# Kernel optimization log

Hardware: AMD Instinct MI355X
Metric: run time of the kernel (lower is better)

The kernel has to match this reference:

```python
import jax, jax.numpy as jnp
import numpy as np

N = 50000   # nodes
E = 400000  # edges per metapath
M = 3       # metapaths
L = 2       # HAN layers
IN = 256    # input feat = hidden*heads so layers stack
H = 4       # heads
DO = 64     # out per head
D = H * DO  # 256


def setup_inputs() -> dict:
    key = jax.random.key(0)
    ks = jax.random.split(key, 12)
    x = jax.random.normal(ks[0], (M, N, IN), jnp.float32)
    src = jax.random.randint(ks[1], (M, E), 0, N, jnp.int32)
    dst = jax.random.randint(ks[2], (M, E), 0, N, jnp.int32)
    W_gat = jax.random.normal(ks[3], (L, M, IN, D), jnp.float32) * 0.06
    attn_l = jax.random.normal(ks[4], (L, M, H, DO), jnp.float32) * 0.1
    attn_r = jax.random.normal(ks[5], (L, M, H, DO), jnp.float32) * 0.1
    bias_gat = jnp.zeros((L, M, D), jnp.float32)
    W1 = jax.random.normal(ks[6], (D, DO), jnp.float32) * 0.06
    b1 = jnp.zeros((DO,), jnp.float32)
    W2 = jax.random.normal(ks[7], (DO, 1), jnp.float32) * 0.1
    Wp = jax.random.normal(ks[8], (D, DO), jnp.float32) * 0.06
    bp = jnp.zeros((DO,), jnp.float32)
    return {"x": x, "W_gat": W_gat, "attn_l": attn_l, "attn_r": attn_r,
            "bias_gat": bias_gat, "W1": W1, "b1": b1, "W2": W2,
            "Wp": Wp, "bp": bp, "src": src, "dst": dst}


def gat_conv(h, src, dst, W, al, ar, bias):
    # h: (N, IN) -> feat: (N, H, DO)
    feat = (h @ W).reshape(N, H, DO)
    el = jnp.einsum('nhd,hd->nh', feat, al)   # (N, H)
    er = jnp.einsum('nhd,hd->nh', feat, ar)   # (N, H)
    e = jax.nn.leaky_relu(el[src] + er[dst], 0.2)  # (E, H)
    # numerically stable edge softmax over incoming edges per dst node
    mx = jax.ops.segment_max(e, dst, num_segments=N)  # (N, H)
    mx = jnp.where(jnp.isfinite(mx), mx, 0.0)         # empty segments
    ex = jnp.exp(e - mx[dst])                         # (E, H)
    denom = jax.ops.segment_sum(ex, dst, num_segments=N)  # (N, H)
    msg = jax.ops.segment_sum(ex[:, :, None] * feat[src], dst, num_segments=N)  # (N,H,DO)
    out = msg / jnp.maximum(denom, 1e-9)[:, :, None]
    out = out + bias.reshape(H, DO)
    return jax.nn.elu(out).reshape(N, D)  # flatten(1)


def reference(x, W_gat, attn_l, attn_r, bias_gat, W1, b1, W2, Wp, bp, src, dst):
    h = [x[i] for i in range(M)]
    for l in range(L):
        h = [gat_conv(h[i], src[i], dst[i], W_gat[l, i], attn_l[l, i],
                      attn_r[l, i], bias_gat[l, i]) for i in range(M)]
    z = jnp.stack(h, axis=1)  # (N, M, D)
    # semantic attention: small MLP -> per-metapath scalar, softmax over M
    w = (jnp.tanh(z @ W1 + b1) @ W2).mean(0)   # (M, 1)
    beta = jax.nn.softmax(w, axis=0)           # (M, 1)
    agg = (z * beta[None]).sum(1)              # (N, D)
    return agg @ Wp + bp                       # (N, DO)
```

## Files before the change

### kernel.cpp

```cpp
#include <hip/hip_runtime.h>

#define NN 50000
#define EE 400000
#define MM 3
#define CHUNK 2048
#define NCHUNK ((NN + CHUNK - 1) / CHUNK)

typedef float f32x4 __attribute__((ext_vector_type(4)));
typedef short s16x8 __attribute__((ext_vector_type(8)));
typedef _Float16 half_t;
typedef _Float16 h16x4 __attribute__((ext_vector_type(4)));

union FU { float f; unsigned u; };

__device__ inline short bfhi(float x) {
    FU c; c.f = x;
    unsigned u = c.u;
    return (short)((u + 0x7fffu + ((u >> 16) & 1u)) >> 16);
}
__device__ inline float bf2f(short h) {
    FU c; c.u = ((unsigned)(unsigned short)h) << 16;
    return c.f;
}
__device__ inline float h2f(short bits) {
    union HU { short s; _Float16 h; } u; u.s = bits; return (float)u.h;
}


__global__ __launch_bounds__(256) void init_kernel(int* counts, float* wsum) {
    int idx = blockIdx.x * 256 + threadIdx.x;
    if (idx < MM * NN) counts[idx] = 0;
    if (idx < MM) wsum[idx] = 0.0f;
}

__global__ __launch_bounds__(256) void hist_kernel(const int* __restrict__ dst,
                                                   int* __restrict__ counts) {
    int m = blockIdx.y;
    int e = blockIdx.x * 256 + threadIdx.x;
    if (e < EE) atomicAdd(&counts[m * NN + dst[m * EE + e]], 1);
}

__global__ __launch_bounds__(256) void scan_partial_kernel(const int* __restrict__ counts,
                                                           int* __restrict__ rp,
                                                           int* __restrict__ bsum) {
    int m = blockIdx.y, ch = blockIdx.x;
    const int* c = counts + m * NN;
    int* r = rp + m * (NN + 1);
    int t = threadIdx.x, lane = t & 63, wave = t >> 6;
    int i0 = ch * CHUNK + t * 8;
    int v[8]; int s = 0;
#pragma unroll
    for (int k = 0; k < 8; ++k) { int i = i0 + k; v[k] = (i < NN) ? c[i] : 0; s += v[k]; }
    int incl = s;
#pragma unroll
    for (int off = 1; off < 64; off <<= 1) {
        int u = __shfl_up(incl, off);
        if (lane >= off) incl += u;
    }
    int excl = incl - s;
    __shared__ int wsh[4];
    if (lane == 63) wsh[wave] = incl;
    __syncthreads();
    int woff = 0;
    for (int w = 0; w < wave; ++w) woff += wsh[w];
    int run = excl + woff;
#pragma unroll
    for (int k = 0; k < 8; ++k) { int i = i0 + k; if (i < NN) r[i] = run; run += v[k]; }
    if (t == 255) bsum[m * NCHUNK + ch] = woff + incl;
}

__global__ __launch_bounds__(256) void scan_top_kernel(int* __restrict__ bsum) {
    int wave = threadIdx.x >> 6, lane = threadIdx.x & 63;
    if (wave < MM) {
        int v = (lane < NCHUNK) ? bsum[wave * NCHUNK + lane] : 0;
        int incl = v;
#pragma unroll
        for (int off = 1; off < 64; off <<= 1) {
            int u = __shfl_up(incl, off);
            if (lane >= off) incl += u;
        }
        if (lane < NCHUNK) bsum[wave * NCHUNK + lane] = incl - v;
    }
}

__global__ __launch_bounds__(256) void scan_add_kernel(const int* __restrict__ bsum,
                                                       int* __restrict__ rp,
                                                       int* __restrict__ cur) {
    int m = blockIdx.y, ch = blockIdx.x;
    int off = bsum[m * NCHUNK + ch];
    int* r = rp + m * (NN + 1);
    int* q = cur + m * (NN + 1);
    int i0 = ch * CHUNK + threadIdx.x * 8;
#pragma unroll
    for (int k = 0; k < 8; ++k) {
        int i = i0 + k;
        if (i < NN) { int val = r[i] + off; r[i] = val; q[i] = val; }
    }
    if (ch == 0 && threadIdx.x == 0) r[NN] = EE;
}

__global__ __launch_bounds__(256) void scatter_kernel(const int* __restrict__ src,
                                                      const int* __restrict__ dst,
                                                      int* __restrict__ cursor,
                                                      long long* __restrict__ spair) {
    int m = blockIdx.y;
    int e = blockIdx.x * 256 + threadIdx.x;
    if (e < EE) {
        int d = dst[m * EE + e];
        int pos = atomicAdd(&cursor[m * (NN + 1) + d], 1);
        long long p = ((long long)d << 32) | (unsigned)src[m * EE + e];
        __builtin_nontemporal_store(p, &spair[(size_t)m * EE + pos]);
    }
}


#define WG_ELEMS (6 * 256 * 256)
#define W_TOT (WG_ELEMS + 128 * 256)

__global__ __launch_bounds__(256) void splitW_kernel(const float* __restrict__ Wg,
                                                     const float* __restrict__ W1,
                                                     const float* __restrict__ Wp,
                                                     short* __restrict__ Whi,
                                                     short* __restrict__ Wlo) {
    int idx = blockIdx.x * 256 + threadIdx.x;
    if (idx >= W_TOT) return;
    float v;
    if (idx < WG_ELEMS) {
        int mat = idx >> 16, rem = idx & 65535;
        int n = rem >> 8, k = rem & 255;
        v = Wg[mat * 65536 + k * 256 + n];
    } else {
        int i2 = idx - WG_ELEMS;
        int n = i2 >> 8, k = i2 & 255;
        v = (n < 64) ? W1[k * 64 + n] : Wp[k * 64 + n - 64];
    }
    short h = bfhi(v);
    Whi[idx] = h;
    Wlo[idx] = bfhi(v - bf2f(h));
}


template<int AMODE>
__global__ __launch_bounds__(256) void mfma_gemm(
    const float* __restrict__ Af, const half_t* __restrict__ A16,
    const short* __restrict__ Wthi, const short* __restrict__ Wtlo,
    half_t* __restrict__ featA,
    const float* __restrict__ alA, const float* __restrict__ arA,
    float* __restrict__ elA, float* __restrict__ erA) {
    __shared__ short Ah[64 * 32], Al[64 * 32], Bh[256 * 32], Bl[256 * 32];
    const int m = blockIdx.y;
    const int t = threadIdx.x;
    const int lane = t & 63;
    const int wn = t >> 6;
    const int row0 = blockIdx.x * 64;
    const float*  A0 = Af + (size_t)m * NN * 256;
    const short*  A1 = (const short*)(A16 + (size_t)m * NN * 256);
    const short*  Bgh = Wthi + (size_t)m * 65536;
    const short*  Bgl = Wtlo + (size_t)m * 65536;
    half_t* Ch = featA + (size_t)m * NN * 256;
    const float* al = alA + m * 256;
    const float* ar = arA + m * 256;
    float* el = elA + (size_t)m * NN * 4;
    float* er = erA + (size_t)m * NN * 4;
    f32x4 acc[4][4] = {};

    const int r = t >> 2, c0 = t & 3;
    const int aoff = r * 32 + ((c0 ^ ((r >> 1) & 3)) << 3);
    const int arow = row0 + r;
    const bool aval = (arow < NN);

    s16x8 praw = {0,0,0,0,0,0,0,0};
    float4 pf0 = make_float4(0.f,0.f,0.f,0.f), pf1 = make_float4(0.f,0.f,0.f,0.f);

    if (AMODE == 1) {
        if (aval) praw = *(const s16x8*)(A1 + (size_t)arow * 256 + c0 * 8);
    } else {
        if (aval) {
            pf0 = *(const float4*)(A0 + (size_t)arow * 256 + c0 * 8);
            pf1 = *(const float4*)(A0 + (size_t)arow * 256 + c0 * 8 + 4);
        }
    }

    for (int k0 = 0; k0 < 256; k0 += 32) {
        {
            float v[8];
            if (AMODE == 1) {
#pragma unroll
                for (int j = 0; j < 8; ++j) v[j] = h2f(praw[j]);
            } else {
                v[0] = pf0.x; v[1] = pf0.y; v[2] = pf0.z; v[3] = pf0.w;
                v[4] = pf1.x; v[5] = pf1.y; v[6] = pf1.z; v[7] = pf1.w;
            }
            s16x8 hh, ll;
#pragma unroll
            for (int j = 0; j < 8; ++j) {
                short hs = bfhi(v[j]);
                hh[j] = hs;
                ll[j] = bfhi(v[j] - bf2f(hs));
            }
            *(s16x8*)&Ah[aoff] = hh;
            *(s16x8*)&Al[aoff] = ll;
        }
#pragma unroll
        for (int u = 0; u < 4; ++u) {
            int n = u * 64 + (t >> 2), c = t & 3;
            s16x8 h = *(const s16x8*)(Bgh + (size_t)n * 256 + k0 + c * 8);
            s16x8 l = *(const s16x8*)(Bgl + (size_t)n * 256 + k0 + c * 8);
            int off = n * 32 + ((c ^ ((n >> 1) & 3)) << 3);
            *(s16x8*)&Bh[off] = h;
            *(s16x8*)&Bl[off] = l;
        }
        __syncthreads();
        if (k0 + 32 < 256) {
            if (AMODE == 1) {
                praw = s16x8{0,0,0,0,0,0,0,0};
                if (aval) praw = *(const s16x8*)(A1 + (size_t)arow * 256 + k0 + 32 + c0 * 8);
            } else {
                pf0 = make_float4(0.f,0.f,0.f,0.f); pf1 = make_float4(0.f,0.f,0.f,0.f);
                if (aval) {
                    pf0 = *(const float4*)(A0 + (size_t)arow * 256 + k0 + 32 + c0 * 8);
                    pf1 = *(const float4*)(A0 + (size_t)arow * 256 + k0 + 32 + c0 * 8 + 4);
                }
            }
        }
        int fr = lane & 15, ac = lane >> 4;
        s16x8 afh[4], afl[4], bfh[4], bfl[4];
#pragma unroll
        for (int i = 0; i < 4; ++i) {
            int rr = i * 16 + fr;
            int off = rr * 32 + ((ac ^ ((rr >> 1) & 3)) << 3);
            afh[i] = *(const s16x8*)&Ah[off];
            afl[i] = *(const s16x8*)&Al[off];
        }
#pragma unroll
        for (int j = 0; j < 4; ++j) {
            int n = wn * 64 + j * 16 + fr;
            int off = n * 32 + ((ac ^ ((n >> 1) & 3)) << 3);
            bfh[j] = *(const s16x8*)&Bh[off];
            bfl[j] = *(const s16x8*)&Bl[off];
        }
#pragma unroll
        for (int i = 0; i < 4; ++i)
#pragma unroll
            for (int j = 0; j < 4; ++j) {
                acc[i][j] = __builtin_amdgcn_mfma_f32_16x16x32_bf16(afh[i], bfh[j], acc[i][j], 0, 0, 0);
                acc[i][j] = __builtin_amdgcn_mfma_f32_16x16x32_bf16(afh[i], bfl[j], acc[i][j], 0, 0, 0);
                acc[i][j] = __builtin_amdgcn_mfma_f32_16x16x32_bf16(afl[i], bfh[j], acc[i][j], 0, 0, 0);
            }
        __syncthreads();
    }

#pragma unroll
    for (int i = 0; i < 4; ++i) {
        int rbase = row0 + i * 16 + (lane >> 4) * 4;
#pragma unroll
        for (int j = 0; j < 4; ++j) {
            int col = wn * 64 + j * 16 + (lane & 15);
#pragma unroll
            for (int q = 0; q < 4; ++q) {
                int row = rbase + q;
                if (row < NN) Ch[(size_t)row * 256 + col] = (half_t)acc[i][j][q];
            }
        }
    }
    float alv[4], arv[4];
#pragma unroll
    for (int j = 0; j < 4; ++j) {
        int col = wn * 64 + j * 16 + (lane & 15);
        alv[j] = al[col];
        arv[j] = ar[col];
    }
#pragma unroll
    for (int i = 0; i < 4; ++i)
#pragma unroll
        for (int q = 0; q < 4; ++q) {
            float ep = acc[i][0][q] * alv[0] + acc[i][1][q] * alv[1]
                     + acc[i][2][q] * alv[2] + acc[i][3][q] * alv[3];
            float rp_ = acc[i][0][q] * arv[0] + acc[i][1][q] * arv[1]
                      + acc[i][2][q] * arv[2] + acc[i][3][q] * arv[3];
#pragma unroll
            for (int msk = 1; msk < 16; msk <<= 1) {
                ep += __shfl_xor(ep, msk);
                rp_ += __shfl_xor(rp_, msk);
            }
            if ((lane & 15) == 0) {
                int row = row0 + i * 16 + (lane >> 4) * 4 + q;
                if (row < NN) {
                    el[row * 4 + wn] = ep;
                    er[row * 4 + wn] = rp_;
                }
            }
        }
}


__global__ __launch_bounds__(256) void sem_gemm(
    const half_t* __restrict__ A16,
    const short* __restrict__ Wthi, const short* __restrict__ Wtlo,
    float* __restrict__ P,
    const float* __restrict__ b1, const float* __restrict__ w2,
    float* __restrict__ wsum,
    int nrows) {
    __shared__ short Ah[128 * 32], Al[128 * 32], Bh[128 * 32], Bl[128 * 32];
    const int t = threadIdx.x;
    const int lane = t & 63;
    const int wave = t >> 6;
    const int wm = wave >> 1, wn = wave & 1;
    const int row0 = blockIdx.x * 128;
    const short* A1 = (const short*)A16;
    f32x4 acc[4][4] = {};

    const int r0 = (t * 2) >> 2, c0 = (t * 2) & 3;
    const int r1 = (t * 2 + 1) >> 2, c1 = (t * 2 + 1) & 3;
    const int aoff0 = r0 * 32 + ((c0 ^ ((r0 >> 1) & 3)) << 3);
    const int aoff1 = r1 * 32 + ((c1 ^ ((r1 >> 1) & 3)) << 3);
    const int arow0 = row0 + r0, arow1 = row0 + r1;

    s16x8 p0 = {0,0,0,0,0,0,0,0}, p1 = {0,0,0,0,0,0,0,0};
    if (arow0 < nrows) p0 = *(const s16x8*)(A1 + (size_t)arow0 * 256 + c0 * 8);
    if (arow1 < nrows) p1 = *(const s16x8*)(A1 + (size_t)arow1 * 256 + c1 * 8);

    for (int k0 = 0; k0 < 256; k0 += 32) {
        {
            s16x8 hh, ll;
#pragma unroll
            for (int j = 0; j < 8; ++j) {
                float v = h2f(p0[j]);
                short hs = bfhi(v);
                hh[j] = hs; ll[j] = bfhi(v - bf2f(hs));
            }
            *(s16x8*)&Ah[aoff0] = hh; *(s16x8*)&Al[aoff0] = ll;
#pragma unroll
            for (int j = 0; j < 8; ++j) {
                float v = h2f(p1[j]);
                short hs = bfhi(v);
                hh[j] = hs; ll[j] = bfhi(v - bf2f(hs));
            }
            *(s16x8*)&Ah[aoff1] = hh; *(s16x8*)&Al[aoff1] = ll;
        }
#pragma unroll
        for (int u = 0; u < 2; ++u) {
            int idx = t * 2 + u;
            int n = idx >> 2, c = idx & 3;
            s16x8 h = *(const s16x8*)(Wthi + (size_t)n * 256 + k0 + c * 8);
            s16x8 l = *(const s16x8*)(Wtlo + (size_t)n * 256 + k0 + c * 8);
            int off = n * 32 + ((c ^ ((n >> 1) & 3)) << 3);
            *(s16x8*)&Bh[off] = h;
            *(s16x8*)&Bl[off] = l;
        }
        __syncthreads();
        if (k0 + 32 < 256) {
            p0 = s16x8{0,0,0,0,0,0,0,0}; p1 = s16x8{0,0,0,0,0,0,0,0};
            if (arow0 < nrows) p0 = *(const s16x8*)(A1 + (size_t)arow0 * 256 + k0 + 32 + c0 * 8);
            if (arow1 < nrows) p1 = *(const s16x8*)(A1 + (size_t)arow1 * 256 + k0 + 32 + c1 * 8);
        }
        int fr = lane & 15, ac = lane >> 4;
        s16x8 afh[4], afl[4], bfh[4], bfl[4];
#pragma unroll
        for (int i = 0; i < 4; ++i) {
            int rr = wm * 64 + i * 16 + fr;
            int off = rr * 32 + ((ac ^ ((rr >> 1) & 3)) << 3);
            afh[i] = *(const s16x8*)&Ah[off];
            afl[i] = *(const s16x8*)&Al[off];
        }
#pragma unroll
        for (int j = 0; j < 4; ++j) {
            int n = wn * 64 + j * 16 + fr;
            int off = n * 32 + ((ac ^ ((n >> 1) & 3)) << 3);
            bfh[j] = *(const s16x8*)&Bh[off];
            bfl[j] = *(const s16x8*)&Bl[off];
        }
#pragma unroll
        for (int i = 0; i < 4; ++i)
#pragma unroll
            for (int j = 0; j < 4; ++j) {
                acc[i][j] = __builtin_amdgcn_mfma_f32_16x16x32_bf16(afh[i], bfh[j], acc[i][j], 0, 0, 0);
                acc[i][j] = __builtin_amdgcn_mfma_f32_16x16x32_bf16(afh[i], bfl[j], acc[i][j], 0, 0, 0);
                acc[i][j] = __builtin_amdgcn_mfma_f32_16x16x32_bf16(afl[i], bfh[j], acc[i][j], 0, 0, 0);
            }
        __syncthreads();
    }

    float* wp = (float*)&Ah[0];
    if (t < 3) wp[t] = 0.f;
    __syncthreads();
    int fr = lane & 15, ac = lane >> 4;
    if (wn == 0) {
        float b1v[4], w2v[4];
#pragma unroll
        for (int j = 0; j < 4; ++j) {
            int col = j * 16 + fr;
            b1v[j] = b1[col];
            w2v[j] = w2[col];
        }
#pragma unroll
        for (int i = 0; i < 4; ++i)
#pragma unroll
            for (int q = 0; q < 4; ++q) {
                float ep = tanhf(acc[i][0][q] + b1v[0]) * w2v[0]
                         + tanhf(acc[i][1][q] + b1v[1]) * w2v[1]
                         + tanhf(acc[i][2][q] + b1v[2]) * w2v[2]
                         + tanhf(acc[i][3][q] + b1v[3]) * w2v[3];
#pragma unroll
                for (int msk = 1; msk < 16; msk <<= 1) ep += __shfl_xor(ep, msk);
                if (fr == 0) {
                    int row = row0 + wm * 64 + i * 16 + ac * 4 + q;
                    if (row < nrows) atomicAdd(&wp[row / NN], ep);
                }
            }
    } else {
#pragma unroll
        for (int i = 0; i < 4; ++i) {
            int rbase = row0 + wm * 64 + i * 16 + ac * 4;
#pragma unroll
            for (int j = 0; j < 4; ++j) {
                int pcol = j * 16 + fr;
#pragma unroll
                for (int q = 0; q < 4; ++q) {
                    int row = rbase + q;
                    if (row < nrows) P[(size_t)row * 64 + pcol] = acc[i][j][q];
                }
            }
        }
    }
    __syncthreads();
    if (t < 3) atomicAdd(&wsum[t], wp[t]);
}


__global__ __launch_bounds__(256) void edge_w_kernel(const long long* __restrict__ spairA,
                                                     const float* __restrict__ elA,
                                                     const float* __restrict__ erA,
                                                     float* __restrict__ wTA) {
    const int m = blockIdx.y;
    int j = blockIdx.x * 256 + threadIdx.x;
    if (j >= EE) return;
    long long p = spairA[(size_t)m * EE + j];
    int s = (int)(unsigned)(p & 0xffffffffLL);
    int d = (int)(p >> 32);
    const float4 e_l = ((const float4*)(elA + (size_t)m * NN * 4))[s];
    const float4 e_r = ((const float4*)(erA + (size_t)m * NN * 4))[d];
    float* wT = wTA + (size_t)m * 4 * EE;
    float e0 = e_l.x + e_r.x; e0 = e0 > 0.f ? e0 : 0.2f * e0;
    float e1 = e_l.y + e_r.y; e1 = e1 > 0.f ? e1 : 0.2f * e1;
    float e2 = e_l.z + e_r.z; e2 = e2 > 0.f ? e2 : 0.2f * e2;
    float e3 = e_l.w + e_r.w; e3 = e3 > 0.f ? e3 : 0.2f * e3;
    wT[0 * EE + j] = __expf(e0);
    wT[1 * EE + j] = __expf(e1);
    wT[2 * EE + j] = __expf(e2);
    wT[3 * EE + j] = __expf(e3);
}


__global__ __launch_bounds__(256) void agg_edges_kernel(const half_t* __restrict__ featA,
                                                        const float* __restrict__ wTA,
                                                        const long long* __restrict__ spairA,
                                                        const int* __restrict__ row_ptrA,
                                                        const float* __restrict__ biasL,
                                                        half_t* __restrict__ HbA) {
    const int m = blockIdx.y;
    const half_t* feat = featA + (size_t)m * NN * 256;
    const int* row_ptr = row_ptrA + (size_t)m * (NN + 1);
    const long long* spair = spairA + (size_t)m * EE;
    const float* bias = biasL + m * 256;
    half_t* out = HbA + (size_t)m * NN * 256;

    int wave = threadIdx.x >> 6;
    int lane = threadIdx.x & 63;
    int n = blockIdx.x * 4 + wave;
    int h = lane >> 4;
    const float* wh = wTA + (size_t)m * 4 * EE + (size_t)h * EE;
    int beg = row_ptr[n], end = row_ptr[n + 1];
    const h16x4* fb = (const h16x4*)feat + lane;
    float a0A = 0.f, a1A = 0.f, a2A = 0.f, a3A = 0.f, dA = 0.f;
    float a0B = 0.f, a1B = 0.f, a2B = 0.f, a3B = 0.f, dB = 0.f;
    float a0C = 0.f, a1C = 0.f, a2C = 0.f, a3C = 0.f, dC = 0.f;
    float a0D = 0.f, a1D = 0.f, a2D = 0.f, a3D = 0.f, dD = 0.f;
    int j = beg;
    for (; j + 3 < end; j += 4) {
        int sA = (int)(unsigned)spair[j];
        int sB = (int)(unsigned)spair[j + 1];
        int sC = (int)(unsigned)spair[j + 2];
        int sD = (int)(unsigned)spair[j + 3];
        float wA = wh[j], wB = wh[j + 1], wC = wh[j + 2], wD = wh[j + 3];
        h16x4 fA = fb[(size_t)sA * 64];
        h16x4 fB = fb[(size_t)sB * 64];
        h16x4 fC = fb[(size_t)sC * 64];
        h16x4 fD = fb[(size_t)sD * 64];
        a0A = fmaf(wA, (float)fA.x, a0A); a1A = fmaf(wA, (float)fA.y, a1A);
        a2A = fmaf(wA, (float)fA.z, a2A); a3A = fmaf(wA, (float)fA.w, a3A); dA += wA;
        a0B = fmaf(wB, (float)fB.x, a0B); a1B = fmaf(wB, (float)fB.y, a1B);
        a2B = fmaf(wB, (float)fB.z, a2B); a3B = fmaf(wB, (float)fB.w, a3B); dB += wB;
        a0C = fmaf(wC, (float)fC.x, a0C); a1C = fmaf(wC, (float)fC.y, a1C);
        a2C = fmaf(wC, (float)fC.z, a2C); a3C = fmaf(wC, (float)fC.w, a3C); dC += wC;
        a0D = fmaf(wD, (float)fD.x, a0D); a1D = fmaf(wD, (float)fD.y, a1D);
        a2D = fmaf(wD, (float)fD.z, a2D); a3D = fmaf(wD, (float)fD.w, a3D); dD += wD;
    }
    for (; j < end; ++j) {
        int s = (int)(unsigned)spair[j];
        float w = wh[j];
        h16x4 f = fb[(size_t)s * 64];
        a0A = fmaf(w, (float)f.x, a0A); a1A = fmaf(w, (float)f.y, a1A);
        a2A = fmaf(w, (float)f.z, a2A); a3A = fmaf(w, (float)f.w, a3A); dA += w;
    }
    float den = fmaxf((dA + dB) + (dC + dD), 1e-9f);
    int col = lane * 4;
    float o0 = ((a0A + a0B) + (a0C + a0D)) / den + bias[col + 0];
    float o1 = ((a1A + a1B) + (a1C + a1D)) / den + bias[col + 1];
    float o2 = ((a2A + a2B) + (a2C + a2D)) / den + bias[col + 2];
    float o3 = ((a3A + a3B) + (a3C + a3D)) / den + bias[col + 3];
    o0 = o0 > 0.f ? o0 : __expf(o0) - 1.0f;
    o1 = o1 > 0.f ? o1 : __expf(o1) - 1.0f;
    o2 = o2 > 0.f ? o2 : __expf(o2) - 1.0f;
    o3 = o3 > 0.f ? o3 : __expf(o3) - 1.0f;
    h16x4 ov; ov.x = (half_t)o0; ov.y = (half_t)o1; ov.z = (half_t)o2; ov.w = (half_t)o3;
    ((h16x4*)(out + (size_t)n * 256))[lane] = ov;
}


__global__ void beta_kernel(const float* __restrict__ wsum, float* __restrict__ beta) {
    if (threadIdx.x == 0 && blockIdx.x == 0) {
        float w0 = wsum[0] / (float)NN, w1 = wsum[1] / (float)NN, w2 = wsum[2] / (float)NN;
        float mx = fmaxf(w0, fmaxf(w1, w2));
        float e0 = __expf(w0 - mx), e1 = __expf(w1 - mx), e2 = __expf(w2 - mx);
        float s = e0 + e1 + e2;
        beta[0] = e0 / s; beta[1] = e1 / s; beta[2] = e2 / s;
    }
}

__global__ __launch_bounds__(256) void combine_out_kernel(const float* __restrict__ P,
                                                          const float* __restrict__ beta,
                                                          const float* __restrict__ bp,
                                                          float* __restrict__ out) {
    int idx4 = blockIdx.x * 256 + threadIdx.x;
    if (idx4 >= NN * 64 / 4) return;
    float b0 = beta[0], b1 = beta[1], b2 = beta[2];
    float4 p0 = ((const float4*)P)[idx4];
    float4 p1 = ((const float4*)P)[idx4 + NN * 16];
    float4 p2 = ((const float4*)P)[idx4 + NN * 32];
    float4 bpv = *(const float4*)(bp + ((idx4 * 4) & 63));
    float4 o;
    o.x = b0 * p0.x + b1 * p1.x + b2 * p2.x + bpv.x;
    o.y = b0 * p0.y + b1 * p1.y + b2 * p2.y + bpv.y;
    o.z = b0 * p0.z + b1 * p1.z + b2 * p2.z + bpv.z;
    o.w = b0 * p0.w + b1 * p1.w + b2 * p2.w + bpv.w;
    ((float4*)out)[idx4] = o;
}


extern "C" void kernel_launch(void* const* d_in, const int* in_sizes, int n_in,
                              void* d_out, int out_size, void* d_ws, size_t ws_size,
                              hipStream_t stream) {
    const float* x        = (const float*)d_in[0];
    const float* W_gat    = (const float*)d_in[1];
    const float* attn_l   = (const float*)d_in[2];
    const float* attn_r   = (const float*)d_in[3];
    const float* bias_gat = (const float*)d_in[4];
    const float* W1       = (const float*)d_in[5];
    const float* b1       = (const float*)d_in[6];
    const float* W2       = (const float*)d_in[7];
    const float* Wp       = (const float*)d_in[8];
    const float* bp       = (const float*)d_in[9];
    const int*   src      = (const int*)d_in[10];
    const int*   dst      = (const int*)d_in[11];
    float* out = (float*)d_out;

    char* ws = (char*)d_ws;
    size_t off = 0;
    auto alloc = [&](size_t bytes) { size_t o = off; off = (off + bytes + 255) & ~(size_t)255; return o; };
    half_t* Hb      = (half_t*)(ws + alloc((size_t)MM * NN * 256 * 2));
    half_t* feat    = (half_t*)(ws + alloc((size_t)MM * NN * 256 * 2));
    float*  P       = (float*)(ws + alloc((size_t)MM * NN * 64 * 4));
    float*  el      = (float*)(ws + alloc((size_t)MM * NN * 4 * 4));
    float*  er      = (float*)(ws + alloc((size_t)MM * NN * 4 * 4));
    int*    counts  = (int*)(ws + alloc((size_t)MM * NN * 4));
    int*    row_ptr = (int*)(ws + alloc((size_t)MM * (NN + 1) * 4));
    int*    cursor  = (int*)(ws + alloc((size_t)MM * (NN + 1) * 4));
    long long* spair = (long long*)(ws + alloc((size_t)MM * EE * 8));
    float*  wT      = (float*)(ws + alloc((size_t)MM * 4 * EE * 4));
    int*    bsum    = (int*)(ws + alloc((size_t)MM * NCHUNK * 4));
    short*  Whi     = (short*)(ws + alloc((size_t)W_TOT * 2));
    short*  Wlo     = (short*)(ws + alloc((size_t)W_TOT * 2));
    float*  wsum    = (float*)(ws + alloc(16));
    float*  beta    = (float*)(ws + alloc(16));

    init_kernel<<<dim3((MM * NN + 255) / 256), 256, 0, stream>>>(counts, wsum);
    hist_kernel<<<dim3((EE + 255) / 256, MM), 256, 0, stream>>>(dst, counts);
    scan_partial_kernel<<<dim3(NCHUNK, MM), 256, 0, stream>>>(counts, row_ptr, bsum);
    scan_top_kernel<<<dim3(1), 256, 0, stream>>>(bsum);
    scan_add_kernel<<<dim3(NCHUNK, MM), 256, 0, stream>>>(bsum, row_ptr, cursor);
    scatter_kernel<<<dim3((EE + 255) / 256, MM), 256, 0, stream>>>(src, dst, cursor, spair);
    splitW_kernel<<<dim3((W_TOT + 255) / 256), 256, 0, stream>>>(W_gat, W1, Wp, Whi, Wlo);

    const int rowTiles = (NN + 63) / 64;

    for (int l = 0; l < 2; ++l) {
        const short* wh = Whi + (size_t)l * MM * 65536;
        const short* wl = Wlo + (size_t)l * MM * 65536;
        const float* alp = attn_l + (size_t)l * MM * 256;
        const float* arp = attn_r + (size_t)l * MM * 256;
        if (l == 0)
            mfma_gemm<0><<<dim3(rowTiles, MM), 256, 0, stream>>>(
                x, nullptr, wh, wl, feat, alp, arp, el, er);
        else
            mfma_gemm<1><<<dim3(rowTiles, MM), 256, 0, stream>>>(
                nullptr, Hb, wh, wl, feat, alp, arp, el, er);
        edge_w_kernel<<<dim3((EE + 255) / 256, MM), 256, 0, stream>>>(spair, el, er, wT);
        agg_edges_kernel<<<dim3(NN / 4, MM), 256, 0, stream>>>(
            feat, wT, spair, row_ptr, bias_gat + (size_t)l * MM * 256, Hb);
    }

    sem_gemm<<<dim3((MM * NN + 127) / 128), 256, 0, stream>>>(
        Hb, Whi + WG_ELEMS, Wlo + WG_ELEMS, P, b1, W2, wsum, MM * NN);
    beta_kernel<<<dim3(1), 64, 0, stream>>>(wsum, beta);
    combine_out_kernel<<<dim3((NN * 16 + 255) / 256), 256, 0, stream>>>(P, beta, bp, out);
}
```

Baseline: 682.7 us.

## Fuse edge weight computation into aggregation and use direct-to-LDS weight loads in GEMM

Removes the separate edge_w_kernel and its wT buffer; the aggregation kernel now recomputes the leaky-relu and exp edge weights from el/er for each gathered source. Each weight is computed 16 times per wave, once per lane of a head, but the global write and read of wT disappear. In the GEMM, the weight matrices are pre-swizzled into the LDS tile layout so B tiles can be copied with global_load_lds, bypassing registers. A-operand prefetch is deepened to two k-blocks ahead.

```diff
diff --git a/kernel.cpp b/kernel.cpp
--- a/kernel.cpp
+++ b/kernel.cpp
@@ -24,6 +24,12 @@
 }
 __device__ inline float h2f(short bits) {
     union HU { short s; _Float16 h; } u; u.s = bits; return (float)u.h;
+}
+
+__device__ inline void glds16(const void* g, void* l) {
+    __builtin_amdgcn_global_load_lds(
+        (const __attribute__((address_space(1))) void*)g,
+        (__attribute__((address_space(3))) void*)l, 16, 0, 0);
 }
 
 
@@ -126,8 +132,16 @@
     if (idx >= W_TOT) return;
     float v;
     if (idx < WG_ELEMS) {
-        int mat = idx >> 16, rem = idx & 65535;
-        int n = rem >> 8, k = rem & 255;
+        int mat = idx >> 16;
+        int rem = idx & 65535;
+        int kb  = rem >> 13;
+        int r2  = rem & 8191;
+        int n   = r2 >> 5;
+        int s5  = r2 & 31;
+        int cc  = s5 >> 3;
+        int jj  = s5 & 7;
+        int c   = cc ^ ((n >> 1) & 3);
+        int k   = kb * 32 + c * 8 + jj;
         v = Wg[mat * 65536 + k * 256 + n];
     } else {
         int i2 = idx - WG_ELEMS;
@@ -155,8 +169,8 @@
     const int row0 = blockIdx.x * 64;
     const float*  A0 = Af + (size_t)m * NN * 256;
     const short*  A1 = (const short*)(A16 + (size_t)m * NN * 256);
-    const short*  Bgh = Wthi + (size_t)m * 65536;
-    const short*  Bgl = Wtlo + (size_t)m * 65536;
+    const char*   BghB = (const char*)(Wthi + (size_t)m * 65536);
+    const char*   BglB = (const char*)(Wtlo + (size_t)m * 65536);
     half_t* Ch = featA + (size_t)m * NN * 256;
     const float* al = alA + m * 256;
     const float* ar = arA + m * 256;
@@ -168,28 +182,34 @@
     const int aoff = r * 32 + ((c0 ^ ((r >> 1) & 3)) << 3);
     const int arow = row0 + r;
     const bool aval = (arow < NN);
-
-    s16x8 praw = {0,0,0,0,0,0,0,0};
-    float4 pf0 = make_float4(0.f,0.f,0.f,0.f), pf1 = make_float4(0.f,0.f,0.f,0.f);
+    const int cb = wn * 4096;
+
+    s16x8 pr0 = {0,0,0,0,0,0,0,0}, pr1 = {0,0,0,0,0,0,0,0};
+    float4 a00 = make_float4(0.f,0.f,0.f,0.f), a01 = a00, a10 = a00, a11 = a00;
 
     if (AMODE == 1) {
-        if (aval) praw = *(const s16x8*)(A1 + (size_t)arow * 256 + c0 * 8);
+        if (aval) {
+            pr0 = *(const s16x8*)(A1 + (size_t)arow * 256 + c0 * 8);
+            pr1 = *(const s16x8*)(A1 + (size_t)arow * 256 + 32 + c0 * 8);
+        }
     } else {
         if (aval) {
-            pf0 = *(const float4*)(A0 + (size_t)arow * 256 + c0 * 8);
-            pf1 = *(const float4*)(A0 + (size_t)arow * 256 + c0 * 8 + 4);
-        }
-    }
-
-    for (int k0 = 0; k0 < 256; k0 += 32) {
+            a00 = *(const float4*)(A0 + (size_t)arow * 256 + c0 * 8);
+            a01 = *(const float4*)(A0 + (size_t)arow * 256 + c0 * 8 + 4);
+            a10 = *(const float4*)(A0 + (size_t)arow * 256 + 32 + c0 * 8);
+            a11 = *(const float4*)(A0 + (size_t)arow * 256 + 32 + c0 * 8 + 4);
+        }
+    }
+
+    for (int kb = 0; kb < 8; ++kb) {
         {
             float v[8];
             if (AMODE == 1) {
 #pragma unroll
-                for (int j = 0; j < 8; ++j) v[j] = h2f(praw[j]);
+                for (int j = 0; j < 8; ++j) v[j] = h2f(pr0[j]);
             } else {
-                v[0] = pf0.x; v[1] = pf0.y; v[2] = pf0.z; v[3] = pf0.w;
-                v[4] = pf1.x; v[5] = pf1.y; v[6] = pf1.z; v[7] = pf1.w;
+                v[0] = a00.x; v[1] = a00.y; v[2] = a00.z; v[3] = a00.w;
+                v[4] = a01.x; v[5] = a01.y; v[6] = a01.z; v[7] = a01.w;
             }
             s16x8 hh, ll;
 #pragma unroll
@@ -201,28 +221,31 @@
             *(s16x8*)&Ah[aoff] = hh;
             *(s16x8*)&Al[aoff] = ll;
         }
-#pragma unroll
-        for (int u = 0; u < 4; ++u) {
-            int n = u * 64 + (t >> 2), c = t & 3;
-            s16x8 h = *(const s16x8*)(Bgh + (size_t)n * 256 + k0 + c * 8);
-            s16x8 l = *(const s16x8*)(Bgl + (size_t)n * 256 + k0 + c * 8);
-            int off = n * 32 + ((c ^ ((n >> 1) & 3)) << 3);
-            *(s16x8*)&Bh[off] = h;
-            *(s16x8*)&Bl[off] = l;
+        if (AMODE == 1) {
+            pr0 = pr1;
+            pr1 = s16x8{0,0,0,0,0,0,0,0};
+            if (kb + 2 < 8 && aval)
+                pr1 = *(const s16x8*)(A1 + (size_t)arow * 256 + (kb + 2) * 32 + c0 * 8);
+        } else {
+            a00 = a10; a01 = a11;
+            a10 = make_float4(0.f,0.f,0.f,0.f); a11 = a10;
+            if (kb + 2 < 8 && aval) {
+                a10 = *(const float4*)(A0 + (size_t)arow * 256 + (kb + 2) * 32 + c0 * 8);
+                a11 = *(const float4*)(A0 + (size_t)arow * 256 + (kb + 2) * 32 + c0 * 8 + 4);
+            }
+        }
+        {
+            const char* sh = BghB + kb * 16384 + cb;
+            const char* sl = BglB + kb * 16384 + cb;
+            char* dh = (char*)&Bh[0] + cb;
+            char* dl = (char*)&Bl[0] + cb;
+#pragma unroll
+            for (int u = 0; u < 4; ++u) {
+                glds16(sh + u * 1024 + lane * 16, dh + u * 1024);
+                glds16(sl + u * 1024 + lane * 16, dl + u * 1024);
+            }
         }
         __syncthreads();
-        if (k0 + 32 < 256) {
-            if (AMODE == 1) {
-                praw = s16x8{0,0,0,0,0,0,0,0};
-                if (aval) praw = *(const s16x8*)(A1 + (size_t)arow * 256 + k0 + 32 + c0 * 8);
-            } else {
-                pf0 = make_float4(0.f,0.f,0.f,0.f); pf1 = make_float4(0.f,0.f,0.f,0.f);
-                if (aval) {
-                    pf0 = *(const float4*)(A0 + (size_t)arow * 256 + k0 + 32 + c0 * 8);
-                    pf1 = *(const float4*)(A0 + (size_t)arow * 256 + k0 + 32 + c0 * 8 + 4);
-                }
-            }
-        }
         int fr = lane & 15, ac = lane >> 4;
         s16x8 afh[4], afl[4], bfh[4], bfl[4];
 #pragma unroll
@@ -428,38 +451,17 @@
 }
 
 
-__global__ __launch_bounds__(256) void edge_w_kernel(const long long* __restrict__ spairA,
-                                                     const float* __restrict__ elA,
-                                                     const float* __restrict__ erA,
-                                                     float* __restrict__ wTA) {
-    const int m = blockIdx.y;
-    int j = blockIdx.x * 256 + threadIdx.x;
-    if (j >= EE) return;
-    long long p = spairA[(size_t)m * EE + j];
-    int s = (int)(unsigned)(p & 0xffffffffLL);
-    int d = (int)(p >> 32);
-    const float4 e_l = ((const float4*)(elA + (size_t)m * NN * 4))[s];
-    const float4 e_r = ((const float4*)(erA + (size_t)m * NN * 4))[d];
-    float* wT = wTA + (size_t)m * 4 * EE;
-    float e0 = e_l.x + e_r.x; e0 = e0 > 0.f ? e0 : 0.2f * e0;
-    float e1 = e_l.y + e_r.y; e1 = e1 > 0.f ? e1 : 0.2f * e1;
-    float e2 = e_l.z + e_r.z; e2 = e2 > 0.f ? e2 : 0.2f * e2;
-    float e3 = e_l.w + e_r.w; e3 = e3 > 0.f ? e3 : 0.2f * e3;
-    wT[0 * EE + j] = __expf(e0);
-    wT[1 * EE + j] = __expf(e1);
-    wT[2 * EE + j] = __expf(e2);
-    wT[3 * EE + j] = __expf(e3);
-}
-
-
 __global__ __launch_bounds__(256) void agg_edges_kernel(const half_t* __restrict__ featA,
-                                                        const float* __restrict__ wTA,
+                                                        const float* __restrict__ elA,
+                                                        const float* __restrict__ erA,
+                                                        const int* __restrict__ row_ptrA,
                                                         const long long* __restrict__ spairA,
-                                                        const int* __restrict__ row_ptrA,
                                                         const float* __restrict__ biasL,
                                                         half_t* __restrict__ HbA) {
     const int m = blockIdx.y;
     const half_t* feat = featA + (size_t)m * NN * 256;
+    const float* el = elA + (size_t)m * NN * 4;
+    const float* er = erA + (size_t)m * NN * 4;
     const int* row_ptr = row_ptrA + (size_t)m * (NN + 1);
     const long long* spair = spairA + (size_t)m * EE;
     const float* bias = biasL + m * 256;
@@ -469,8 +471,8 @@
     int lane = threadIdx.x & 63;
     int n = blockIdx.x * 4 + wave;
     int h = lane >> 4;
-    const float* wh = wTA + (size_t)m * 4 * EE + (size_t)h * EE;
     int beg = row_ptr[n], end = row_ptr[n + 1];
+    float ern = er[n * 4 + h];
     const h16x4* fb = (const h16x4*)feat + lane;
     float a0A = 0.f, a1A = 0.f, a2A = 0.f, a3A = 0.f, dA = 0.f;
     float a0B = 0.f, a1B = 0.f, a2B = 0.f, a3B = 0.f, dB = 0.f;
@@ -482,7 +484,10 @@
         int sB = (int)(unsigned)spair[j + 1];
         int sC = (int)(unsigned)spair[j + 2];
         int sD = (int)(unsigned)spair[j + 3];
-        float wA = wh[j], wB = wh[j + 1], wC = wh[j + 2], wD = wh[j + 3];
+        float eA = el[sA * 4 + h] + ern; eA = eA > 0.f ? eA : 0.2f * eA; float wA = __expf(eA);
+        float eB = el[sB * 4 + h] + ern; eB = eB > 0.f ? eB : 0.2f * eB; float wB = __expf(eB);
+        float eC = el[sC * 4 + h] + ern; eC = eC > 0.f ? eC : 0.2f * eC; float wC = __expf(eC);
+        float eD = el[sD * 4 + h] + ern; eD = eD > 0.f ? eD : 0.2f * eD; float wD = __expf(eD);
         h16x4 fA = fb[(size_t)sA * 64];
         h16x4 fB = fb[(size_t)sB * 64];
         h16x4 fC = fb[(size_t)sC * 64];
@@ -498,7 +503,9 @@
     }
     for (; j < end; ++j) {
         int s = (int)(unsigned)spair[j];
-        float w = wh[j];
+        float e = el[s * 4 + h] + ern;
+        e = e > 0.f ? e : 0.2f * e;
+        float w = __expf(e);
         h16x4 f = fb[(size_t)s * 64];
         a0A = fmaf(w, (float)f.x, a0A); a1A = fmaf(w, (float)f.y, a1A);
         a2A = fmaf(w, (float)f.z, a2A); a3A = fmaf(w, (float)f.w, a3A); dA += w;
@@ -577,7 +584,6 @@
     int*    row_ptr = (int*)(ws + alloc((size_t)MM * (NN + 1) * 4));
     int*    cursor  = (int*)(ws + alloc((size_t)MM * (NN + 1) * 4));
     long long* spair = (long long*)(ws + alloc((size_t)MM * EE * 8));
-    float*  wT      = (float*)(ws + alloc((size_t)MM * 4 * EE * 4));
     int*    bsum    = (int*)(ws + alloc((size_t)MM * NCHUNK * 4));
     short*  Whi     = (short*)(ws + alloc((size_t)W_TOT * 2));
     short*  Wlo     = (short*)(ws + alloc((size_t)W_TOT * 2));
@@ -605,9 +611,8 @@
         else
             mfma_gemm<1><<<dim3(rowTiles, MM), 256, 0, stream>>>(
                 nullptr, Hb, wh, wl, feat, alp, arp, el, er);
-        edge_w_kernel<<<dim3((EE + 255) / 256, MM), 256, 0, stream>>>(spair, el, er, wT);
         agg_edges_kernel<<<dim3(NN / 4, MM), 256, 0, stream>>>(
-            feat, wT, spair, row_ptr, bias_gat + (size_t)l * MM * 256, Hb);
+            feat, el, er, row_ptr, spair, bias_gat + (size_t)l * MM * 256, Hb);
     }
 
     sem_gemm<<<dim3((MM * NN + 127) / 128), 256, 0, stream>>>(
```

Measured after the change: 657.7 us. 3.7% less time.
